# Optimization experiments

Measured on AMD Instinct MI355X. Metric: run time of the kernel, lower is better.

Reference implementation:

```python
import jax, jax.numpy as jnp
import numpy as np
from jax import lax

DN = ('NCHW', 'OIHW', 'NCHW')

def conv(x, w, b, stride=1):
    y = lax.conv_general_dilated(x, w, window_strides=(stride, stride),
                                 padding='VALID', dimension_numbers=DN)
    return y + b[None, :, None, None]

def maxpool(x, k=3, s=2):
    return lax.reduce_window(x, -jnp.inf, lax.max,
                             (1, 1, k, k), (1, 1, s, s), 'VALID')

def setup_inputs() -> dict:
    key = jax.random.key(0)
    ks = jax.random.split(key, 7)
    B = 2048
    x = jax.random.normal(ks[0], (B, 1, 28, 28), dtype=jnp.float32)
    w1 = jax.random.normal(ks[1], (64, 1, 3, 3), dtype=jnp.float32)
    b1 = jax.random.normal(ks[2], (64,), dtype=jnp.float32)
    w2 = jax.random.normal(ks[3], (64, 64, 3, 3), dtype=jnp.float32)
    b2 = jax.random.normal(ks[4], (64,), dtype=jnp.float32)
    w3 = jax.random.normal(ks[5], (10, 64, 4, 4), dtype=jnp.float32)
    b3 = jax.random.normal(ks[6], (10,), dtype=jnp.float32)
    return {"x": x, "w1": w1, "b1": b1, "w2": w2, "b2": b2, "w3": w3, "b3": b3}

def reference(x, w1, b1, w2, b2, w3, b3):
    h = conv(x, w1, b1)            # [B,64,26,26]
    h = maxpool(h)                 # [B,64,12,12]
    h = jnp.maximum(h, 0.0)
    h = conv(h, w2, b2)            # [B,64,10,10]
    h = maxpool(h)                 # [B,64,4,4]
    h = jnp.maximum(h, 0.0)
    h = conv(h, w3, b3)            # [B,10,1,1]
    return h.reshape(h.shape[0], -1)  # [B,10]
```

## Files before the change

kernel.cpp:

```cpp
#include <hip/hip_runtime.h>


typedef __attribute__((ext_vector_type(8))) short short8;
typedef __attribute__((ext_vector_type(16))) float f32x16;

__device__ inline short f2bf(float f) {
    union { float f; unsigned u; } v; v.f = f;
    unsigned r = (v.u + 0x7FFFu + ((v.u >> 16) & 1u)) >> 16;
    return (short)r;
}

__global__ __launch_bounds__(256) void prep_w2(const float* __restrict__ w2,
                                               short* __restrict__ w2r) {
    int i = blockIdx.x * 256 + threadIdx.x;
    if (i >= 36864) return;
    int s = i >> 12, cout = (i >> 6) & 63, cin = i & 63;
    w2r[i] = f2bf(w2[cout * 576 + cin * 9 + s]);
}

__global__ __launch_bounds__(256) void convnet_fused(
    const float* __restrict__ x,
    const float* __restrict__ w1,
    const float* __restrict__ b1,
    const short* __restrict__ w2r,
    const float* __restrict__ b2,
    const float* __restrict__ w3,
    const float* __restrict__ b3,
    float* __restrict__ out)
{
    __shared__ float lds_f[7488];
    short* h1t  = (short*)lds_f;
    float* cbuf = lds_f;
    float* h2t  = lds_f + 6464;
    float* prt  = lds_f;

    const int n_img = blockIdx.x;
    const int t = threadIdx.x;
    const int c = t >> 2;
    const int q = t & 3;

    const float* img_g = x + (size_t)n_img * 784;

    {
        const int oy = (q >> 1) * 6, ox = (q & 1) * 6;
        const int iy0 = 2 * oy, ix0 = 2 * ox;
        float w[9];
        #pragma unroll
        for (int k = 0; k < 9; ++k) w[k] = w1[c * 9 + k];
        const float bias = b1[c];

        float rows[3][16];
        {
            const float* s0 = img_g + iy0 * 28 + ix0;
            const float* s1 = img_g + (iy0 + 1) * 28 + ix0;
            #pragma unroll
            for (int m = 0; m < 4; ++m) {
                *(float4*)(rows[0] + 4 * m) = *(const float4*)(s0 + 4 * m);
                *(float4*)(rows[1] + 4 * m) = *(const float4*)(s1 + 4 * m);
            }
        }
        float cm[3][6];
        #pragma unroll
        for (int r = 0; r < 13; ++r) {
            {
                const float* s2 = img_g + (iy0 + r + 2) * 28 + ix0;
                float* dst = rows[(r + 2) % 3];
                #pragma unroll
                for (int m = 0; m < 4; ++m)
                    *(float4*)(dst + 4 * m) = *(const float4*)(s2 + 4 * m);
            }
            const float* r0 = rows[r % 3];
            const float* r1 = rows[(r + 1) % 3];
            const float* r2 = rows[(r + 2) % 3];
            #pragma unroll
            for (int px = 0; px < 6; ++px) cm[r % 3][px] = -1e30f;
            #pragma unroll
            for (int xx = 0; xx < 13; ++xx) {
                float a = bias;
                #pragma unroll
                for (int j = 0; j < 3; ++j) {
                    a += r0[xx + j] * w[j];
                    a += r1[xx + j] * w[3 + j];
                    a += r2[xx + j] * w[6 + j];
                }
                if ((xx & 1) == 0) {
                    if (xx >= 2 && xx <= 12) cm[r % 3][xx / 2 - 1] = fmaxf(cm[r % 3][xx / 2 - 1], a);
                    if (xx <= 10)            cm[r % 3][xx / 2]     = fmaxf(cm[r % 3][xx / 2], a);
                } else {
                    cm[r % 3][xx / 2] = fmaxf(cm[r % 3][xx / 2], a);
                }
            }
            if (r >= 2 && (r & 1) == 0) {
                const int py = r / 2 - 1;
                #pragma unroll
                for (int px = 0; px < 6; ++px) {
                    float m = fmaxf(fmaxf(cm[0][px], cm[1][px]), cm[2][px]);
                    h1t[((oy + py) * 12 + ox + px) * 72 + c] = f2bf(fmaxf(m, 0.0f));
                }
            }
        }
    }
    __syncthreads();

    const int wv = t >> 6, lane = t & 63;
    const int mtile = wv & 1, npair = wv >> 1;
    const int col32 = lane & 31, khalf = lane >> 5;
    {
        int base_el[2];
        #pragma unroll
        for (int nt2 = 0; nt2 < 2; ++nt2) {
            int n = (npair * 2 + nt2) * 32 + col32;
            if (n > 99) n = 99;
            int y = n / 10, xx = n - y * 10;
            base_el[nt2] = (y * 12 + xx) * 72;
        }
        f32x16 acc[2];
        #pragma unroll
        for (int nt2 = 0; nt2 < 2; ++nt2)
            #pragma unroll
            for (int r = 0; r < 16; ++r) acc[nt2][r] = 0.0f;

        #pragma unroll
        for (int step = 0; step < 36; ++step) {
            const int s = step >> 2;
            const int cinb = (step & 3) * 16 + khalf * 8;
            const short8 a = *(const short8*)(w2r + s * 4096 + (mtile * 32 + col32) * 64 + cinb);
            const int ky = s / 3, kx = s - ky * 3;
            const int toff = (ky * 12 + kx) * 72 + cinb;
            #pragma unroll
            for (int nt2 = 0; nt2 < 2; ++nt2) {
                const short8 b = *(const short8*)(h1t + base_el[nt2] + toff);
                acc[nt2] = __builtin_amdgcn_mfma_f32_32x32x16_bf16(a, b, acc[nt2], 0, 0, 0);
            }
        }
        __syncthreads();
        #pragma unroll
        for (int nt2 = 0; nt2 < 2; ++nt2) {
            const int n = (npair * 2 + nt2) * 32 + col32;
            if (n < 100) {
                #pragma unroll
                for (int reg = 0; reg < 16; ++reg) {
                    const int row = (reg & 3) + 8 * (reg >> 2) + 4 * khalf;
                    const int cout = mtile * 32 + row;
                    cbuf[cout * 101 + n] = acc[nt2][reg] + b2[cout];
                }
            }
        }
    }
    __syncthreads();

    {
        const float* cb = cbuf + c * 101;
        #pragma unroll
        for (int k = 0; k < 4; ++k) {
            const int pos = q * 4 + k;
            const int py = pos >> 2, px = pos & 3;
            float m = -1e30f;
            #pragma unroll
            for (int a = 0; a < 3; ++a)
                #pragma unroll
                for (int b = 0; b < 3; ++b)
                    m = fmaxf(m, cb[(2 * py + a) * 10 + (2 * px + b)]);
            h2t[pos * 64 + c] = fmaxf(m, 0.0f);
        }
    }
    __syncthreads();

    if (t < 160) {
        const int o = t >> 4, g = t & 15;
        const float* w3o = w3 + o * 1024 + g * 64;
        float wr[4][16];
        #pragma unroll
        for (int cc = 0; cc < 4; ++cc)
            #pragma unroll
            for (int m = 0; m < 4; ++m)
                *(float4*)(wr[cc] + 4 * m) = *(const float4*)(w3o + cc * 16 + 4 * m);
        float s = 0.0f;
        #pragma unroll
        for (int pos = 0; pos < 16; ++pos) {
            const float4 hv = *(const float4*)(h2t + pos * 64 + g * 4);
            s += hv.x * wr[0][pos] + hv.y * wr[1][pos] + hv.z * wr[2][pos] + hv.w * wr[3][pos];
        }
        prt[t] = s;
    }
    __syncthreads();
    if (t < 10) {
        float s = b3[t];
        #pragma unroll
        for (int g = 0; g < 16; ++g) s += prt[t * 16 + g];
        out[(size_t)n_img * 10 + t] = s;
    }
}

extern "C" void kernel_launch(void* const* d_in, const int* in_sizes, int n_in,
                              void* d_out, int out_size, void* d_ws, size_t ws_size,
                              hipStream_t stream) {
    const float* x  = (const float*)d_in[0];
    const float* w1 = (const float*)d_in[1];
    const float* b1 = (const float*)d_in[2];
    const float* w2 = (const float*)d_in[3];
    const float* b2 = (const float*)d_in[4];
    const float* w3 = (const float*)d_in[5];
    const float* b3 = (const float*)d_in[6];
    float* out = (float*)d_out;
    short* w2r = (short*)d_ws;

    const int B = in_sizes[0] / 784;
    prep_w2<<<144, 256, 0, stream>>>(w2, w2r);
    convnet_fused<<<B, 256, 0, stream>>>(x, w1, b1, w2r, b2, w3, b3, out);
}
```

Baseline: 130.5 us.

## Stage input image in LDS and retile conv2 MFMA to 16x16x32 with 7 N-tiles

Copies each 28x28 input image into shared memory once, so the conv1 row loads come from LDS rather than repeated global reads. Replaces the conv2 32x32x16 MFMA tiling (2 M-tiles x 2 N-pairs per wave) with 16x16x32 MFMAs, where each wave owns 16 output channels and 7 N-tiles that cover all 100 positions. This cuts the padded N work from 128 to 112 columns and reuses each A fragment across 7 MFMAs. In exchange it holds more accumulator and B-load registers per wave, and the extra LDS region for the image may alias other buffers.

```diff
diff --git a/kernel.cpp b/kernel.cpp
--- a/kernel.cpp
+++ b/kernel.cpp
@@ -2,7 +2,7 @@
 
 
 typedef __attribute__((ext_vector_type(8))) short short8;
-typedef __attribute__((ext_vector_type(16))) float f32x16;
+typedef __attribute__((ext_vector_type(4))) float f32x4;
 
 __device__ inline short f2bf(float f) {
     union { float f; unsigned u; } v; v.f = f;
@@ -30,6 +30,7 @@
 {
     __shared__ float lds_f[7488];
     short* h1t  = (short*)lds_f;
+    float* img  = lds_f + 5184;
     float* cbuf = lds_f;
     float* h2t  = lds_f + 6464;
     float* prt  = lds_f;
@@ -40,6 +41,8 @@
     const int q = t & 3;
 
     const float* img_g = x + (size_t)n_img * 784;
+    for (int i = t; i < 784; i += 256) img[i] = img_g[i];
+    __syncthreads();
 
     {
         const int oy = (q >> 1) * 6, ox = (q & 1) * 6;
@@ -51,8 +54,8 @@
 
         float rows[3][16];
         {
-            const float* s0 = img_g + iy0 * 28 + ix0;
-            const float* s1 = img_g + (iy0 + 1) * 28 + ix0;
+            const float* s0 = img + iy0 * 28 + ix0;
+            const float* s1 = img + (iy0 + 1) * 28 + ix0;
             #pragma unroll
             for (int m = 0; m < 4; ++m) {
                 *(float4*)(rows[0] + 4 * m) = *(const float4*)(s0 + 4 * m);
@@ -60,10 +63,11 @@
             }
         }
         float cm[3][6];
+
         #pragma unroll
         for (int r = 0; r < 13; ++r) {
             {
-                const float* s2 = img_g + (iy0 + r + 2) * 28 + ix0;
+                const float* s2 = img + (iy0 + r + 2) * 28 + ix0;
                 float* dst = rows[(r + 2) % 3];
                 #pragma unroll
                 for (int m = 0; m < 4; ++m)
@@ -103,46 +107,41 @@
     __syncthreads();
 
     const int wv = t >> 6, lane = t & 63;
-    const int mtile = wv & 1, npair = wv >> 1;
-    const int col32 = lane & 31, khalf = lane >> 5;
+    const int quad = lane >> 4, mrow = lane & 15;
     {
-        int base_el[2];
-        #pragma unroll
-        for (int nt2 = 0; nt2 < 2; ++nt2) {
-            int n = (npair * 2 + nt2) * 32 + col32;
-            if (n > 99) n = 99;
+        int base_el[7];
+        #pragma unroll
+        for (int nt = 0; nt < 7; ++nt) {
+            int n = nt * 16 + mrow; if (n > 99) n = 99;
             int y = n / 10, xx = n - y * 10;
-            base_el[nt2] = (y * 12 + xx) * 72;
-        }
-        f32x16 acc[2];
-        #pragma unroll
-        for (int nt2 = 0; nt2 < 2; ++nt2)
-            #pragma unroll
-            for (int r = 0; r < 16; ++r) acc[nt2][r] = 0.0f;
-
-        #pragma unroll
-        for (int step = 0; step < 36; ++step) {
-            const int s = step >> 2;
-            const int cinb = (step & 3) * 16 + khalf * 8;
-            const short8 a = *(const short8*)(w2r + s * 4096 + (mtile * 32 + col32) * 64 + cinb);
+            base_el[nt] = (y * 12 + xx) * 72;
+        }
+        f32x4 acc[7];
+        #pragma unroll
+        for (int nt = 0; nt < 7; ++nt) acc[nt] = (f32x4){0.f, 0.f, 0.f, 0.f};
+
+        #pragma unroll
+        for (int ks = 0; ks < 18; ++ks) {
+            const int s = ks >> 1, h = ks & 1;
             const int ky = s / 3, kx = s - ky * 3;
-            const int toff = (ky * 12 + kx) * 72 + cinb;
-            #pragma unroll
-            for (int nt2 = 0; nt2 < 2; ++nt2) {
-                const short8 b = *(const short8*)(h1t + base_el[nt2] + toff);
-                acc[nt2] = __builtin_amdgcn_mfma_f32_32x32x16_bf16(a, b, acc[nt2], 0, 0, 0);
+            const short8 a = *(const short8*)(w2r + s * 4096 + (wv * 16 + mrow) * 64
+                                              + h * 32 + quad * 8);
+            #pragma unroll
+            for (int nt = 0; nt < 7; ++nt) {
+                const short8 b = *(const short8*)(h1t + base_el[nt]
+                                                  + (ky * 12 + kx) * 72 + h * 32 + quad * 8);
+                acc[nt] = __builtin_amdgcn_mfma_f32_16x16x32_bf16(a, b, acc[nt], 0, 0, 0);
             }
         }
         __syncthreads();
         #pragma unroll
-        for (int nt2 = 0; nt2 < 2; ++nt2) {
-            const int n = (npair * 2 + nt2) * 32 + col32;
+        for (int nt = 0; nt < 7; ++nt) {
+            const int n = nt * 16 + mrow;
             if (n < 100) {
                 #pragma unroll
-                for (int reg = 0; reg < 16; ++reg) {
-                    const int row = (reg & 3) + 8 * (reg >> 2) + 4 * khalf;
-                    const int cout = mtile * 32 + row;
-                    cbuf[cout * 101 + n] = acc[nt2][reg] + b2[cout];
+                for (int r = 0; r < 4; ++r) {
+                    const int co = wv * 16 + quad * 4 + r;
+                    cbuf[co * 101 + n] = acc[nt][r] + b2[co];
                 }
             }
         }
```

New measurement: 112.0 us. -14.1%, faster.
